# Kernel tuning notes

Hardware: AMD Instinct MI355X
Metric: run time of the kernel (lower is better)

## Reference

```python
import jax, jax.numpy as jnp
import numpy as np
from jax import lax

# TT-conv configuration (matches init_kwargs)
M = (4, 8, 8)        # in_c_modes, prod = 256
O = (4, 8, 8)        # out_c_modes, prod = 256
R = (16, 16, 16, 1)  # ranks with trailing 1 appended as in the module
B, H, W = 8, 64, 64
IN_C = int(np.prod(M))


def setup_inputs() -> dict:
    key = jax.random.key(0)
    ks = jax.random.split(key, 6)
    X = jax.random.normal(ks[0], (B, IN_C, H, W), jnp.float32)
    conv_w = jax.random.normal(ks[1], (R[0], 1, 3, 3), jnp.float32) * 0.3
    conv_b = jax.random.normal(ks[2], (R[0],), jnp.float32) * 0.05
    def xavier(k, shape):
        fan_in, fan_out = shape[1], shape[0]
        std = (2.0 / (fan_in + fan_out)) ** 0.5
        return jax.random.normal(k, shape, jnp.float32) * std
    core1 = xavier(ks[3], (O[0] * R[1], R[0] * M[0]))  # (64, 64)
    core2 = xavier(ks[4], (O[1] * R[2], R[1] * M[1]))  # (128, 128)
    core3 = xavier(ks[5], (O[2] * R[3], R[2] * M[2]))  # (8, 128)
    return {"X": X, "conv_w": conv_w, "conv_b": conv_b,
            "core1": core1, "core2": core2, "core3": core3}


def reference(X, conv_w, conv_b, core1, core2, core3):
    b, in_c, h, w = X.shape
    # core0: depth-agnostic 1->r0 conv applied per input channel
    y = lax.conv_general_dilated(
        X.reshape(-1, 1, h, w), conv_w,
        window_strides=(1, 1), padding=((1, 1), (1, 1)),
        dimension_numbers=("NCHW", "OIHW", "NCHW"))
    y = y + conv_b[None, :, None, None]          # (B*in_c, r0, h, w)
    hh, ww = y.shape[-2:]
    # (B, m1, m2, m3, r0, h, w): in_c factored row-major, m1 most significant
    y = y.reshape(b, M[0], M[1], M[2], R[0], hh, ww)
    # TT cores reshaped (o_i, r_{i+1}, r_i, m_i)
    G1 = core1.reshape(O[0], R[1], R[0], M[0])
    G2 = core2.reshape(O[1], R[2], R[1], M[1])
    G3 = core3.reshape(O[2], R[3], R[2], M[2])
    # Full TT contraction chain collapsed into one einsum; s (=r3) has size 1.
    out = jnp.einsum("bijkrhw,auri,cvuj,dsvk->bacdhw",
                     y, G1, G2, G3, optimize=True)
    # channel order (o1, o2, o3) with o3 fastest, as in the torch module
    return out.reshape(b, O[0] * O[1] * O[2], hh, ww)
```

## Files before the change

### kernel.cpp

```cpp
#include <hip/hip_runtime.h>
#include <hip/hip_bf16.h>
#include <stdint.h>

typedef __attribute__((ext_vector_type(8))) short short8;
typedef __attribute__((ext_vector_type(4))) float f32x4;

#define XP_BYTES   17842176
#define XP_PAD     1024
#define OFF_W9     (XP_BYTES + XP_PAD)
#define W9_BYTES   (8*9*256*32*2)
#define OFF_BIAS   (OFF_W9 + W9_BYTES)

__device__ __forceinline__ short f2bf(float f) {
  __hip_bfloat16 h = __float2bfloat16(f);
  return *reinterpret_cast<short*>(&h);
}

__device__ __forceinline__ void gl_lds16(const void* g, void* l) {
  __builtin_amdgcn_global_load_lds(
      (const __attribute__((address_space(1))) void*)g,
      (__attribute__((address_space(3))) void*)l, 16, 0, 0);
}

__global__ void k_prep(const float* __restrict__ X,
                       const float* __restrict__ core1,
                       const float* __restrict__ core2,
                       const float* __restrict__ core3,
                       const float* __restrict__ convw,
                       const float* __restrict__ convb,
                       short* __restrict__ Xp,
                       short* __restrict__ W9, float* __restrict__ bias) {
  if (blockIdx.x < 256) {
    __shared__ float H2s[1024];
    __shared__ float red[256];
    const int o = blockIdx.x, c = threadIdx.x;
    const int a = o >> 6, c2 = (o >> 3) & 7, d = o & 7;
#pragma unroll
    for (int p = 0; p < 4; ++p) {
      int idx = c + (p << 8);
      int k = idx & 7, j = (idx >> 3) & 7, u = idx >> 6;
      float s = 0.f;
#pragma unroll
      for (int v = 0; v < 16; ++v)
        s += core2[(c2 * 16 + v) * 128 + u * 8 + j] * core3[d * 128 + v * 8 + k];
      H2s[idx] = s;
    }
    __syncthreads();
    const int i = c >> 6, j = (c >> 3) & 7, k = c & 7;
    float Wr[16];
#pragma unroll
    for (int r = 0; r < 16; ++r) Wr[r] = 0.f;
    for (int u = 0; u < 16; ++u) {
      float h = H2s[u * 64 + j * 8 + k];
      const float* c1 = core1 + (a * 16 + u) * 64 + i;
#pragma unroll
      for (int r = 0; r < 16; ++r) Wr[r] += c1[r * 4] * h;
    }
    const int cb = c >> 5, cl = c & 31, g = cl >> 3, pos = cl & 7;
    const int gslot = g ^ (o & 3);
#pragma unroll
    for (int t = 0; t < 9; ++t) {
      float s = 0.f;
#pragma unroll
      for (int r = 0; r < 16; ++r) s += Wr[r] * convw[r * 9 + t];
      W9[((size_t)((cb * 9 + t) * 256 + o)) * 32 + gslot * 8 + pos] = f2bf(s);
    }
    float s = 0.f;
#pragma unroll
    for (int r = 0; r < 16; ++r) s += Wr[r] * convb[r];
    red[c] = s;
    __syncthreads();
    for (int st = 128; st > 0; st >>= 1) {
      if (c < st) red[c] += red[c + st];
      __syncthreads();
    }
    if (c == 0) bias[o] = red[0];
    return;
  }
  const int p = blockIdx.x - 256;
  const int cb = p / 528, rem = p % 528;
  const int b = rem / 66, yp = rem % 66;
  const int t = threadIdx.x;
  short* rowp = Xp + ((size_t)((b * 8 + cb) * 66 + yp)) * 264 * 8;
  const short8 z = (short8){0, 0, 0, 0, 0, 0, 0, 0};
  if (yp == 0 || yp == 65) {
    *(short8*)(rowp + t * 8) = z;
    if (t < 8) *(short8*)(rowp + ((256 + t) * 8)) = z;
    return;
  }
  __shared__ __align__(16) short Ls[264 * 8];
  *(short8*)&Ls[t * 8] = z;
  if (t < 8) *(short8*)&Ls[(256 + t) * 8] = z;
  __syncthreads();
  const int x = t & 63, sub = t >> 6, xp = x + 1, y = yp - 1;
  const int gslot = sub ^ ((xp >> 1) & 3);
  const float* src = X + ((size_t)(b * 256 + cb * 32 + sub * 8) * 64 + y) * 64 + x;
  short8 v;
#pragma unroll
  for (int k = 0; k < 8; ++k) v[k] = f2bf(src[(size_t)k * 4096]);
  *(short8*)&Ls[(xp * 4 + gslot) * 8] = v;
  __syncthreads();
  *(short8*)(rowp + t * 8) = *(const short8*)&Ls[t * 8];
  if (t < 8) *(short8*)(rowp + (256 + t) * 8) = *(const short8*)&Ls[(256 + t) * 8];
}

__global__ __launch_bounds__(512, 1) void k_gemm(
    const short* __restrict__ Xp, const short* __restrict__ W9,
    const float* __restrict__ bias, float* __restrict__ out) {
  __shared__ __align__(16) short XL[2][38400];

  const int tid  = threadIdx.x;
  const int lane = tid & 63;
  const int wv   = tid >> 6;
  const int l15  = lane & 15;
  const int gl   = lane >> 4;
  const int h0    = blockIdx.x << 4;
  const int oBase = blockIdx.y << 5;
  const int b     = blockIdx.z;
  const int r0    = wv << 1;

  int xoff[4][3];
#pragma unroll
  for (int xr = 0; xr < 4; ++xr)
#pragma unroll
    for (int dx = 0; dx < 3; ++dx)
      xoff[xr][dx] = ((r0 + xr) * 66 + l15 + dx) * 32 +
                     ((gl ^ (((l15 + dx) >> 1) & 3)) << 3);

  const int laneW = (oBase + l15) * 32 + ((gl ^ (l15 & 3)) << 3);

  f32x4 acc[2][2][4];
#pragma unroll
  for (int rr = 0; rr < 2; ++rr)
#pragma unroll
    for (int io = 0; io < 2; ++io)
#pragma unroll
      for (int ip = 0; ip < 4; ++ip)
        acc[rr][io][ip] = (f32x4){0.f, 0.f, 0.f, 0.f};

#define STAGE(CB, BUF)                                                     \
  {                                                                        \
    const size_t xb = ((size_t)(((b << 3) + (CB)) * 66 + h0) * 66) << 5;   \
    _Pragma("unroll 1")                                                    \
    for (int q = wv; q < 75; q += 8)                                       \
      gl_lds16(Xp + xb + (q << 9) + (lane << 3), &XL[BUF][q << 9]);        \
  }

  STAGE(0, 0);

  for (int cb = 0; cb < 8; ++cb) {
    const short* Wc = W9 + cb * 73728 + laneW;
    short8 af[9][2];
#pragma unroll
    for (int t = 0; t < 9; ++t)
#pragma unroll
      for (int io = 0; io < 2; ++io)
        af[t][io] = *(const short8*)&Wc[t * 8192 + (io << 9)];
    __builtin_amdgcn_sched_barrier(0);

    __syncthreads();

    if (cb < 7) STAGE(cb + 1, (cb + 1) & 1);
    __builtin_amdgcn_sched_barrier(0);

    const short* XLc = &XL[cb & 1][0];
    short8 bfr[2][4];

#define LOADS(BUF, DX, IP)                                                 \
  {                                                                        \
    _Pragma("unroll")                                                      \
    for (int xr = 0; xr < 4; ++xr)                                         \
      bfr[BUF][xr] = *(const short8*)&XLc[xoff[xr][DX] + ((IP) << 9)];     \
  }

    LOADS(0, 0, 0);
#pragma unroll
    for (int s = 0; s < 12; ++s) {
      const int dx = s >> 2, ip = s & 3, buf = s & 1;
      if (s < 11) LOADS(buf ^ 1, (s + 1) >> 2, (s + 1) & 3);
      __builtin_amdgcn_sched_barrier(0);
      __builtin_amdgcn_s_setprio(1);
#pragma unroll
      for (int dy = 0; dy < 3; ++dy) {
        const int t = dy * 3 + dx;
#pragma unroll
        for (int io = 0; io < 2; ++io) {
          acc[0][io][ip] = __builtin_amdgcn_mfma_f32_16x16x32_bf16(
              af[t][io], bfr[buf][dy], acc[0][io][ip], 0, 0, 0);
          acc[1][io][ip] = __builtin_amdgcn_mfma_f32_16x16x32_bf16(
              af[t][io], bfr[buf][dy + 1], acc[1][io][ip], 0, 0, 0);
        }
      }
      __builtin_amdgcn_s_setprio(0);
    }
#undef LOADS
  }
#undef STAGE

#pragma unroll
  for (int rr = 0; rr < 2; ++rr) {
    const int h = h0 + r0 + rr;
#pragma unroll
    for (int io = 0; io < 2; ++io) {
#pragma unroll
      for (int r = 0; r < 4; ++r) {
        const int oG = oBase + (io << 4) + (gl << 2) + r;
        const float bv = bias[oG];
        float* op = out + (((size_t)((b << 8) + oG)) << 12) + (h << 6);
#pragma unroll
        for (int ip = 0; ip < 4; ++ip)
          op[(ip << 4) + l15] = acc[rr][io][ip][r] + bv;
      }
    }
  }
}

extern "C" void kernel_launch(void* const* d_in, const int* in_sizes, int n_in,
                              void* d_out, int out_size, void* d_ws, size_t ws_size,
                              hipStream_t stream) {
  (void)in_sizes; (void)n_in; (void)out_size; (void)ws_size;
  const float* X     = (const float*)d_in[0];
  const float* convw = (const float*)d_in[1];
  const float* convb = (const float*)d_in[2];
  const float* core1 = (const float*)d_in[3];
  const float* core2 = (const float*)d_in[4];
  const float* core3 = (const float*)d_in[5];
  float* out = (float*)d_out;
  char*  ws  = (char*)d_ws;

  short* Xp   = (short*)ws;
  short* W9   = (short*)(ws + OFF_W9);
  float* bias = (float*)(ws + OFF_BIAS);

  k_prep<<<4480, 256, 0, stream>>>(X, core1, core2, core3, convw, convb,
                                   Xp, W9, bias);
  k_gemm<<<dim3(4, 8, 8), 512, 0, stream>>>(Xp, W9, bias, out);
}
```

Baseline: 131.7 us.

## Switch GEMM to 32x32x16 MFMA with new Xp layout and tiling

Rewrites the implicit-GEMM conv kernel to use 32x32x16 bf16 MFMA tiles instead of 16x16x32. It changes the Xp workspace layout to per-8-channel slots and drops the XOR swizzle. Tiles become 8 rows by 64 output channels per block, and the next channel block is staged in two halves interleaved with compute. The goal is fewer LDS reads per MFMA and better reuse, at the cost of a smaller LDS footprint per stage and possible bank conflicts from the unswizzled layout.

```diff
diff --git a/kernel.cpp b/kernel.cpp
--- a/kernel.cpp
+++ b/kernel.cpp
@@ -3,7 +3,7 @@
 #include <stdint.h>
 
 typedef __attribute__((ext_vector_type(8))) short short8;
-typedef __attribute__((ext_vector_type(4))) float f32x4;
+typedef __attribute__((ext_vector_type(16))) float f32x16;
 
 #define XP_BYTES   17842176
 #define XP_PAD     1024
@@ -56,14 +56,13 @@
 #pragma unroll
       for (int r = 0; r < 16; ++r) Wr[r] += c1[r * 4] * h;
     }
-    const int cb = c >> 5, cl = c & 31, g = cl >> 3, pos = cl & 7;
-    const int gslot = g ^ (o & 3);
+    const int cb = c >> 5, cl = c & 31;
 #pragma unroll
     for (int t = 0; t < 9; ++t) {
       float s = 0.f;
 #pragma unroll
       for (int r = 0; r < 16; ++r) s += Wr[r] * convw[r * 9 + t];
-      W9[((size_t)((cb * 9 + t) * 256 + o)) * 32 + gslot * 8 + pos] = f2bf(s);
+      W9[((size_t)((cb * 9 + t) * 256 + o)) * 32 + cl] = f2bf(s);
     }
     float s = 0.f;
 #pragma unroll
@@ -81,11 +80,17 @@
   const int cb = p / 528, rem = p % 528;
   const int b = rem / 66, yp = rem % 66;
   const int t = threadIdx.x;
-  short* rowp = Xp + ((size_t)((b * 8 + cb) * 66 + yp)) * 264 * 8;
   const short8 z = (short8){0, 0, 0, 0, 0, 0, 0, 0};
+  const size_t reg0 = (size_t)(b * 8 + cb) * 4;
   if (yp == 0 || yp == 65) {
-    *(short8*)(rowp + t * 8) = z;
-    if (t < 8) *(short8*)(rowp + ((256 + t) * 8)) = z;
+    {
+      const int slot = t / 66, x = t % 66;
+      *(short8*)(Xp + (((reg0 + slot) * 66 + yp) * 66 + x) * 8) = z;
+    }
+    if (t < 8) {
+      const int g_ = 256 + t, slot = g_ / 66, x = g_ % 66;
+      *(short8*)(Xp + (((reg0 + slot) * 66 + yp) * 66 + x) * 8) = z;
+    }
     return;
   }
   __shared__ __align__(16) short Ls[264 * 8];
@@ -93,123 +98,140 @@
   if (t < 8) *(short8*)&Ls[(256 + t) * 8] = z;
   __syncthreads();
   const int x = t & 63, sub = t >> 6, xp = x + 1, y = yp - 1;
-  const int gslot = sub ^ ((xp >> 1) & 3);
   const float* src = X + ((size_t)(b * 256 + cb * 32 + sub * 8) * 64 + y) * 64 + x;
   short8 v;
 #pragma unroll
   for (int k = 0; k < 8; ++k) v[k] = f2bf(src[(size_t)k * 4096]);
-  *(short8*)&Ls[(xp * 4 + gslot) * 8] = v;
+  *(short8*)&Ls[(sub * 66 + xp) * 8] = v;
   __syncthreads();
-  *(short8*)(rowp + t * 8) = *(const short8*)&Ls[t * 8];
-  if (t < 8) *(short8*)(rowp + (256 + t) * 8) = *(const short8*)&Ls[(256 + t) * 8];
+  {
+    const int slot = t / 66, xc = t % 66;
+    *(short8*)(Xp + (((reg0 + slot) * 66 + yp) * 66 + xc) * 8) =
+        *(const short8*)&Ls[t * 8];
+  }
+  if (t < 8) {
+    const int g_ = 256 + t, slot = g_ / 66, xc = g_ % 66;
+    *(short8*)(Xp + (((reg0 + slot) * 66 + yp) * 66 + xc) * 8) =
+        *(const short8*)&Ls[g_ * 8];
+  }
 }
 
 __global__ __launch_bounds__(512, 1) void k_gemm(
     const short* __restrict__ Xp, const short* __restrict__ W9,
     const float* __restrict__ bias, float* __restrict__ out) {
-  __shared__ __align__(16) short XL[2][38400];
+  __shared__ __align__(16) short XL[2][22528];
 
   const int tid  = threadIdx.x;
   const int lane = tid & 63;
   const int wv   = tid >> 6;
-  const int l15  = lane & 15;
-  const int gl   = lane >> 4;
-  const int h0    = blockIdx.x << 4;
-  const int oBase = blockIdx.y << 5;
+  const int l31  = lane & 31;
+  const int h5   = lane >> 5;
+  const int hp   = wv >> 1;
+  const int xh   = wv & 1;
+  const int h0    = blockIdx.x << 3;
+  const int oBase = blockIdx.y << 6;
   const int b     = blockIdx.z;
-  const int r0    = wv << 1;
-
-  int xoff[4][3];
-#pragma unroll
-  for (int xr = 0; xr < 4; ++xr)
-#pragma unroll
-    for (int dx = 0; dx < 3; ++dx)
-      xoff[xr][dx] = ((r0 + xr) * 66 + l15 + dx) * 32 +
-                     ((gl ^ (((l15 + dx) >> 1) & 3)) << 3);
-
-  const int laneW = (oBase + l15) * 32 + ((gl ^ (l15 & 3)) << 3);
-
-  f32x4 acc[2][2][4];
+  const int x0w   = xh << 5;
+
+  const int bof0 = (h5) * 5632 + ((hp * 132) + x0w + l31) * 8;
+  const int bof1 = (2 + h5) * 5632 + ((hp * 132) + x0w + l31) * 8;
+  const int wbase = (oBase + l31) * 32 + h5 * 8;
+
+  f32x16 acc[2][2];
 #pragma unroll
   for (int rr = 0; rr < 2; ++rr)
 #pragma unroll
     for (int io = 0; io < 2; ++io)
 #pragma unroll
-      for (int ip = 0; ip < 4; ++ip)
-        acc[rr][io][ip] = (f32x4){0.f, 0.f, 0.f, 0.f};
-
-#define STAGE(CB, BUF)                                                     \
-  {                                                                        \
-    const size_t xb = ((size_t)(((b << 3) + (CB)) * 66 + h0) * 66) << 5;   \
-    _Pragma("unroll 1")                                                    \
-    for (int q = wv; q < 75; q += 8)                                       \
-      gl_lds16(Xp + xb + (q << 9) + (lane << 3), &XL[BUF][q << 9]);        \
-  }
-
-  STAGE(0, 0);
+      for (int r = 0; r < 16; ++r) acc[rr][io][r] = 0.f;
+
+#define STG(CB, BUF, QLO, QHI)                                                \
+  {                                                                           \
+    _Pragma("unroll 1")                                                       \
+    for (int q = (QLO) + wv; q < (QHI); q += 8) {                             \
+      const int slot = q / 11, i = q % 11;                                    \
+      const short* src = Xp +                                                 \
+          ((((size_t)(b * 8 + (CB)) * 4 + slot) * 66 + h0) * 66               \
+           + (i << 6) + lane) * 8;                                            \
+      gl_lds16(src, &XL[BUF][slot * 5632 + (i << 9) + (lane << 3)]);          \
+    }                                                                         \
+  }
+
+  STG(0, 0, 0, 44);
 
   for (int cb = 0; cb < 8; ++cb) {
-    const short* Wc = W9 + cb * 73728 + laneW;
+    const short* Wc = W9 + cb * 73728 + wbase;
     short8 af[9][2];
 #pragma unroll
     for (int t = 0; t < 9; ++t)
 #pragma unroll
       for (int io = 0; io < 2; ++io)
-        af[t][io] = *(const short8*)&Wc[t * 8192 + (io << 9)];
+        af[t][io] = *(const short8*)&Wc[t * 8192 + (io << 10)];
     __builtin_amdgcn_sched_barrier(0);
 
     __syncthreads();
 
-    if (cb < 7) STAGE(cb + 1, (cb + 1) & 1);
+    if (cb < 7) STG(cb + 1, (cb + 1) & 1, 0, 22);
     __builtin_amdgcn_sched_barrier(0);
 
     const short* XLc = &XL[cb & 1][0];
     short8 bfr[2][4];
 
-#define LOADS(BUF, DX, IP)                                                 \
-  {                                                                        \
-    _Pragma("unroll")                                                      \
-    for (int xr = 0; xr < 4; ++xr)                                         \
-      bfr[BUF][xr] = *(const short8*)&XLc[xoff[xr][DX] + ((IP) << 9)];     \
-  }
-
-    LOADS(0, 0, 0);
-#pragma unroll
-    for (int s = 0; s < 12; ++s) {
-      const int dx = s >> 2, ip = s & 3, buf = s & 1;
-      if (s < 11) LOADS(buf ^ 1, (s + 1) >> 2, (s + 1) & 3);
-      __builtin_amdgcn_sched_barrier(0);
-      __builtin_amdgcn_s_setprio(1);
-#pragma unroll
-      for (int dy = 0; dy < 3; ++dy) {
-        const int t = dy * 3 + dx;
-#pragma unroll
-        for (int io = 0; io < 2; ++io) {
-          acc[0][io][ip] = __builtin_amdgcn_mfma_f32_16x16x32_bf16(
-              af[t][io], bfr[buf][dy], acc[0][io][ip], 0, 0, 0);
-          acc[1][io][ip] = __builtin_amdgcn_mfma_f32_16x16x32_bf16(
-              af[t][io], bfr[buf][dy + 1], acc[1][io][ip], 0, 0, 0);
-        }
-      }
-      __builtin_amdgcn_s_setprio(0);
-    }
+#define LOADS(SET, BOF, DX)                                                   \
+  {                                                                           \
+    _Pragma("unroll")                                                         \
+    for (int xr = 0; xr < 4; ++xr)                                            \
+      bfr[SET][xr] = *(const short8*)&XLc[(BOF) + (xr * 66 + (DX)) * 8];      \
+  }
+
+#define MM(SET, DX)                                                           \
+  {                                                                           \
+    __builtin_amdgcn_s_setprio(1);                                            \
+    _Pragma("unroll")                                                         \
+    for (int dy = 0; dy < 3; ++dy)                                            \
+      _Pragma("unroll")                                                       \
+      for (int rr = 0; rr < 2; ++rr)                                          \
+        _Pragma("unroll")                                                     \
+        for (int io = 0; io < 2; ++io)                                        \
+          acc[rr][io] = __builtin_amdgcn_mfma_f32_32x32x16_bf16(              \
+              af[dy * 3 + (DX)][io], bfr[SET][rr + dy], acc[rr][io], 0, 0, 0);\
+    __builtin_amdgcn_s_setprio(0);                                            \
+  }
+
+    LOADS(0, bof0, 0);
+    LOADS(1, bof0, 1); __builtin_amdgcn_sched_barrier(0); MM(0, 0);
+    LOADS(0, bof0, 2); __builtin_amdgcn_sched_barrier(0); MM(1, 1);
+    __builtin_amdgcn_sched_barrier(0);                    MM(0, 2);
+
+#pragma unroll
+    for (int t = 0; t < 9; ++t)
+#pragma unroll
+      for (int io = 0; io < 2; ++io)
+        af[t][io] = *(const short8*)&Wc[16 + t * 8192 + (io << 10)];
+    __builtin_amdgcn_sched_barrier(0);
+    if (cb < 7) STG(cb + 1, (cb + 1) & 1, 22, 44);
+    __builtin_amdgcn_sched_barrier(0);
+
+    LOADS(0, bof1, 0);
+    LOADS(1, bof1, 1); __builtin_amdgcn_sched_barrier(0); MM(0, 0);
+    LOADS(0, bof1, 2); __builtin_amdgcn_sched_barrier(0); MM(1, 1);
+    __builtin_amdgcn_sched_barrier(0);                    MM(0, 2);
+#undef MM
 #undef LOADS
   }
-#undef STAGE
+#undef STG
 
 #pragma unroll
   for (int rr = 0; rr < 2; ++rr) {
-    const int h = h0 + r0 + rr;
+    const int h = h0 + hp * 2 + rr;
 #pragma unroll
     for (int io = 0; io < 2; ++io) {
 #pragma unroll
-      for (int r = 0; r < 4; ++r) {
-        const int oG = oBase + (io << 4) + (gl << 2) + r;
-        const float bv = bias[oG];
-        float* op = out + (((size_t)((b << 8) + oG)) << 12) + (h << 6);
-#pragma unroll
-        for (int ip = 0; ip < 4; ++ip)
-          op[(ip << 4) + l15] = acc[rr][io][ip][r] + bv;
+      for (int r = 0; r < 16; ++r) {
+        const int orow = (r & 3) + ((r >> 2) << 3) + (h5 << 2);
+        const int oG = oBase + (io << 5) + orow;
+        out[(((size_t)(b * 256 + oG)) * 64 + h) * 64 + x0w + l31] =
+            acc[rr][io][r] + bias[oG];
       }
     }
   }
@@ -234,5 +256,5 @@
 
   k_prep<<<4480, 256, 0, stream>>>(X, core1, core2, core3, convw, convb,
                                    Xp, W9, bias);
-  k_gemm<<<dim3(4, 8, 8), 512, 0, stream>>>(Xp, W9, bias, out);
-}
+  k_gemm<<<dim3(8, 4, 8), 512, 0, stream>>>(Xp, W9, bias, out);
+}
```

Measured after the change: 153.4 us. 16.5% more time.

## Retile conv-GEMM into smaller 256-thread blocks with split-x tiles and staged loads

Applied to the files above, without the earlier changes.

Restructures the implicit-GEMM kernel from 256 blocks of 512 threads (16 rows × 32 outputs) to 1024 blocks of 256 threads, each covering 4 rows × 32 columns × 64 output channels. The LDS tile shrinks so three blocks can co-reside per CU. Weight fragments are now loaded per dx in three register sets, and the next channel-block's global->LDS staging is split into three chunks interleaved with the MFMA phases. The aim is to fill all CUs, raise occupancy and hide load latency. The cost is more halo re-reads from the x split and more blocks re-reading W9.

```diff
diff --git a/kernel.cpp b/kernel.cpp
--- a/kernel.cpp
+++ b/kernel.cpp
@@ -104,113 +104,132 @@
   if (t < 8) *(short8*)(rowp + (256 + t) * 8) = *(const short8*)&Ls[(256 + t) * 8];
 }
 
-__global__ __launch_bounds__(512, 1) void k_gemm(
+__global__ __launch_bounds__(256, 3) void k_gemm(
     const short* __restrict__ Xp, const short* __restrict__ W9,
     const float* __restrict__ bias, float* __restrict__ out) {
-  __shared__ __align__(16) short XL[2][38400];
+  __shared__ __align__(16) short XL[2][9216];
 
   const int tid  = threadIdx.x;
   const int lane = tid & 63;
   const int wv   = tid >> 6;
   const int l15  = lane & 15;
   const int gl   = lane >> 4;
-  const int h0    = blockIdx.x << 4;
-  const int oBase = blockIdx.y << 5;
+  const int h0    = blockIdx.x << 2;
+  const int o4    = blockIdx.y & 3;
+  const int xh    = blockIdx.y >> 2;
+  const int oBase = o4 << 6;
+  const int x0    = xh << 5;
+  const int xlo   = xh ? 18 : 0;
   const int b     = blockIdx.z;
-  const int r0    = wv << 1;
-
-  int xoff[4][3];
-#pragma unroll
-  for (int xr = 0; xr < 4; ++xr)
-#pragma unroll
-    for (int dx = 0; dx < 3; ++dx)
-      xoff[xr][dx] = ((r0 + xr) * 66 + l15 + dx) * 32 +
-                     ((gl ^ (((l15 + dx) >> 1) & 3)) << 3);
-
+
+  int xoff[3][3];
+#pragma unroll
+  for (int dy = 0; dy < 3; ++dy)
+#pragma unroll
+    for (int dx = 0; dx < 3; ++dx) {
+      const int x = x0 + l15 + dx;
+      xoff[dy][dx] = ((wv + dy) * 192 + (x - xlo) * 4 + (gl ^ ((x >> 1) & 3))) * 8;
+    }
   const int laneW = (oBase + l15) * 32 + ((gl ^ (l15 & 3)) << 3);
 
-  f32x4 acc[2][2][4];
-#pragma unroll
-  for (int rr = 0; rr < 2; ++rr)
-#pragma unroll
-    for (int io = 0; io < 2; ++io)
-#pragma unroll
-      for (int ip = 0; ip < 4; ++ip)
-        acc[rr][io][ip] = (f32x4){0.f, 0.f, 0.f, 0.f};
-
-#define STAGE(CB, BUF)                                                     \
-  {                                                                        \
-    const size_t xb = ((size_t)(((b << 3) + (CB)) * 66 + h0) * 66) << 5;   \
-    _Pragma("unroll 1")                                                    \
-    for (int q = wv; q < 75; q += 8)                                       \
-      gl_lds16(Xp + xb + (q << 9) + (lane << 3), &XL[BUF][q << 9]);        \
-  }
-
-  STAGE(0, 0);
+  f32x4 acc[4][2];
+#pragma unroll
+  for (int io = 0; io < 4; ++io)
+#pragma unroll
+    for (int ip = 0; ip < 2; ++ip)
+      acc[io][ip] = (f32x4){0.f, 0.f, 0.f, 0.f};
+
+#define STG(CB, BUF, QLO, QHI)                                                \
+  {                                                                           \
+    _Pragma("unroll 1")                                                       \
+    for (int q = (QLO) + wv; q < (QHI); q += 4) {                             \
+      const int row = q / 3, cc = q % 3;                                      \
+      const short* src = Xp +                                                 \
+          (((size_t)((b << 3) + (CB)) * 66 + h0 + row) * 264                  \
+           + (xlo << 2) + (cc << 6) + lane) * 8;                              \
+      gl_lds16(src, &XL[BUF][(q << 9) + (lane << 3)]);                        \
+    }                                                                         \
+  }
+
+#define AF(DST, CB, DX)                                                       \
+  {                                                                           \
+    const short* Wc = W9 + (size_t)(CB) * 73728 + laneW;                      \
+    _Pragma("unroll")                                                         \
+    for (int dy = 0; dy < 3; ++dy)                                            \
+      _Pragma("unroll")                                                       \
+      for (int io = 0; io < 4; ++io)                                          \
+        DST[dy][io] = *(const short8*)&Wc[(dy * 3 + (DX)) * 8192 + io * 512]; \
+  }
+
+#define BFR(DX)                                                               \
+  {                                                                           \
+    _Pragma("unroll")                                                         \
+    for (int dy = 0; dy < 3; ++dy)                                            \
+      _Pragma("unroll")                                                       \
+      for (int ip = 0; ip < 2; ++ip)                                          \
+        bfr[dy][ip] = *(const short8*)&XLc[xoff[dy][DX] + (ip << 9)];         \
+  }
+
+#define MM(AFR)                                                               \
+  {                                                                           \
+    __builtin_amdgcn_s_setprio(1);                                            \
+    _Pragma("unroll")                                                         \
+    for (int dy = 0; dy < 3; ++dy)                                            \
+      _Pragma("unroll")                                                       \
+      for (int io = 0; io < 4; ++io)                                          \
+        _Pragma("unroll")                                                     \
+        for (int ip = 0; ip < 2; ++ip)                                        \
+          acc[io][ip] = __builtin_amdgcn_mfma_f32_16x16x32_bf16(              \
+              AFR[dy][io], bfr[dy][ip], acc[io][ip], 0, 0, 0);                \
+    __builtin_amdgcn_s_setprio(0);                                            \
+  }
+
+  STG(0, 0, 0, 18);
+
+  short8 af0[3][4], af1[3][4], af2[3][4];
+  short8 bfr[3][2];
 
   for (int cb = 0; cb < 8; ++cb) {
-    const short* Wc = W9 + cb * 73728 + laneW;
-    short8 af[9][2];
-#pragma unroll
-    for (int t = 0; t < 9; ++t)
-#pragma unroll
-      for (int io = 0; io < 2; ++io)
-        af[t][io] = *(const short8*)&Wc[t * 8192 + (io << 9)];
-    __builtin_amdgcn_sched_barrier(0);
-
+    AF(af0, cb, 0);
+    __builtin_amdgcn_sched_barrier(0);
     __syncthreads();
 
-    if (cb < 7) STAGE(cb + 1, (cb + 1) & 1);
-    __builtin_amdgcn_sched_barrier(0);
-
     const short* XLc = &XL[cb & 1][0];
-    short8 bfr[2][4];
-
-#define LOADS(BUF, DX, IP)                                                 \
-  {                                                                        \
-    _Pragma("unroll")                                                      \
-    for (int xr = 0; xr < 4; ++xr)                                         \
-      bfr[BUF][xr] = *(const short8*)&XLc[xoff[xr][DX] + ((IP) << 9)];     \
-  }
-
-    LOADS(0, 0, 0);
-#pragma unroll
-    for (int s = 0; s < 12; ++s) {
-      const int dx = s >> 2, ip = s & 3, buf = s & 1;
-      if (s < 11) LOADS(buf ^ 1, (s + 1) >> 2, (s + 1) & 3);
-      __builtin_amdgcn_sched_barrier(0);
-      __builtin_amdgcn_s_setprio(1);
-#pragma unroll
-      for (int dy = 0; dy < 3; ++dy) {
-        const int t = dy * 3 + dx;
-#pragma unroll
-        for (int io = 0; io < 2; ++io) {
-          acc[0][io][ip] = __builtin_amdgcn_mfma_f32_16x16x32_bf16(
-              af[t][io], bfr[buf][dy], acc[0][io][ip], 0, 0, 0);
-          acc[1][io][ip] = __builtin_amdgcn_mfma_f32_16x16x32_bf16(
-              af[t][io], bfr[buf][dy + 1], acc[1][io][ip], 0, 0, 0);
-        }
-      }
-      __builtin_amdgcn_s_setprio(0);
-    }
-#undef LOADS
-  }
-#undef STAGE
-
-#pragma unroll
-  for (int rr = 0; rr < 2; ++rr) {
-    const int h = h0 + r0 + rr;
-#pragma unroll
-    for (int io = 0; io < 2; ++io) {
-#pragma unroll
-      for (int r = 0; r < 4; ++r) {
-        const int oG = oBase + (io << 4) + (gl << 2) + r;
-        const float bv = bias[oG];
-        float* op = out + (((size_t)((b << 8) + oG)) << 12) + (h << 6);
-#pragma unroll
-        for (int ip = 0; ip < 4; ++ip)
-          op[(ip << 4) + l15] = acc[rr][io][ip][r] + bv;
-      }
+    const int nb = (cb + 1) & 1;
+
+    if (cb < 7) STG(cb + 1, nb, 0, 6);
+    __builtin_amdgcn_sched_barrier(0);
+    AF(af1, cb, 1);
+    __builtin_amdgcn_sched_barrier(0);
+    if (cb < 7) STG(cb + 1, nb, 6, 12);
+    __builtin_amdgcn_sched_barrier(0);
+
+    BFR(0); MM(af0);
+
+    AF(af2, cb, 2);
+    __builtin_amdgcn_sched_barrier(0);
+    if (cb < 7) STG(cb + 1, nb, 12, 18);
+    __builtin_amdgcn_sched_barrier(0);
+
+    BFR(1); MM(af1);
+    BFR(2); MM(af2);
+  }
+#undef MM
+#undef BFR
+#undef AF
+#undef STG
+
+  const int h = h0 + wv;
+#pragma unroll
+  for (int io = 0; io < 4; ++io) {
+#pragma unroll
+    for (int r = 0; r < 4; ++r) {
+      const int oG = oBase + (io << 4) + (gl << 2) + r;
+      const float bv = bias[oG];
+      float* op = out + (((size_t)((b << 8) + oG)) << 12) + (h << 6) + x0;
+#pragma unroll
+      for (int ip = 0; ip < 2; ++ip)
+        op[(ip << 4) + l15] = acc[io][ip][r] + bv;
     }
   }
 }
@@ -234,5 +253,5 @@
 
   k_prep<<<4480, 256, 0, stream>>>(X, core1, core2, core3, convw, convb,
                                    Xp, W9, bias);
-  k_gemm<<<dim3(4, 8, 8), 512, 0, stream>>>(Xp, W9, bias, out);
-}
+  k_gemm<<<dim3(16, 8, 8), 256, 0, stream>>>(Xp, W9, bias, out);
+}
```

After: 150.4 us. 1.14x slower.
